# Kernel tuning notes

Hardware: AMD Instinct MI355X
Metric: run time of the kernel (lower is better)

Reference implementation:

```python
import jax, jax.numpy as jnp
import numpy as np

N_NODES = 50000
N_EDGES = 800000
NFEAT = 128
NHID = 64
NLAYER = 3
BN_EPS = 1e-5


def _bn(h, gamma, beta):
    # BatchNorm1d, training-mode batch statistics (biased variance)
    mu = jnp.mean(h, axis=0)
    var = jnp.mean((h - mu) ** 2, axis=0)
    return gamma * (h - mu) * jax.lax.rsqrt(var + BN_EPS) + beta


def setup_inputs() -> dict:
    key = jax.random.key(0)
    ks = jax.random.split(key, 8)
    x = jax.random.normal(ks[0], (N_NODES, NFEAT), dtype=jnp.float32)
    edge_index = jax.random.randint(ks[1], (2, N_EDGES), 0, N_NODES, dtype=jnp.int64)
    # transform: Linear(nfeat, nhid) with bias, then BN
    W_t = jax.random.normal(ks[2], (NFEAT, NHID), dtype=jnp.float32) / np.sqrt(NFEAT)
    b_t = jnp.zeros((NHID,), dtype=jnp.float32)
    g_t = jnp.ones((NHID,), dtype=jnp.float32)
    bb_t = jnp.zeros((NHID,), dtype=jnp.float32)
    # per-layer GIN MLPs (bias=False) and BN affine params, stacked over layers
    W1 = jax.random.normal(ks[3], (NLAYER, NHID, NHID), dtype=jnp.float32) / np.sqrt(NHID)
    W2 = jax.random.normal(ks[4], (NLAYER, NHID, NHID), dtype=jnp.float32) / np.sqrt(NHID)
    gamma = jnp.ones((NLAYER, NHID), dtype=jnp.float32)
    beta = jnp.zeros((NLAYER, NHID), dtype=jnp.float32)
    return {"x": x, "edge_index": edge_index, "W_t": W_t, "b_t": b_t,
            "g_t": g_t, "bb_t": bb_t, "W1": W1, "W2": W2,
            "gamma": gamma, "beta": beta}


def reference(x, edge_index, W_t, b_t, g_t, bb_t, W1, W2, gamma, beta):
    src, dst = edge_index[0], edge_index[1]
    # input transform: Linear + BN
    h = _bn(x @ W_t + b_t, g_t, bb_t)
    for i in range(NLAYER):
        # dropout p=0 -> identity
        # GINConv (eps=0): (1+eps)*h + sum_{j->i} h_j, then 2-layer MLP
        agg = h + jax.ops.segment_sum(h[src], dst, num_segments=N_NODES)
        h = jax.nn.relu(agg @ W1[i]) @ W2[i]
        h = jax.nn.relu(h)
        h = _bn(h, gamma[i], beta[i])
    # per-graph boolean-mask split is a pure partition of rows; return full matrix
    return h
```

## Files before the change

kernel.cpp:

```cpp
#include <hip/hip_runtime.h>

#define NND 50000
#define NED 800000
#define NF  128
#define NH  64
#define BN_EPS 1e-5
#define NCOPY 8
#define SCB  256
#define NSB  ((NND + SCB - 1) / SCB)
#define XNODES (NND / 8)
#define FCH  196
#define NT   782
#define PGRID (FCH * 8)

#define WS_HB     0
#define WS_AGG    6400000
#define WS_STATS  12800000
#define WS_DEG    (WS_STATS + 4*NCOPY*128*4)
#define WS_OFFS   (WS_DEG + NND*4)
#define WS_CUR    (WS_OFFS + (NND+4)*4)
#define WS_PARTS  (WS_CUR + NND*4)
#define WS_ESRC   (WS_PARTS + 256*4)

__device__ __forceinline__ unsigned bfrn(float x) {
    unsigned u = __float_as_uint(x);
    return (u + 0x7fffu + ((u >> 16) & 1u)) >> 16;
}
__device__ __forceinline__ unsigned pk(float lo, float hi) {
    return bfrn(lo) | (bfrn(hi) << 16);
}
__device__ __forceinline__ void upadd(unsigned u, float& lo, float& hi) {
    lo += __uint_as_float(u << 16);
    hi += __uint_as_float(u & 0xffff0000u);
}
__device__ __forceinline__ float ulo(unsigned u) { return __uint_as_float(u << 16); }
__device__ __forceinline__ float uhi(unsigned u) { return __uint_as_float(u & 0xffff0000u); }

__device__ __forceinline__ void bn_derive(const float* __restrict__ st, int c,
                                          const float* __restrict__ g,
                                          const float* __restrict__ b,
                                          float& sc, float& sh) {
    float sum = 0.f, ssq = 0.f;
#pragma unroll
    for (int cp = 0; cp < NCOPY; ++cp) {
        sum += st[cp * 128 + c];
        ssq += st[cp * 128 + 64 + c];
    }
    double mu  = (double)sum / (double)NND;
    double var = (double)ssq / (double)NND - mu * mu;
    if (var < 0.0) var = 0.0;
    double rs = 1.0 / sqrt(var + BN_EPS);
    double scd = (double)g[c] * rs;
    sc = (float)scd;
    sh = (float)((double)b[c] - mu * scd);
}

__global__ __launch_bounds__(256) void k_dtf(const int* __restrict__ dst,
                                             int* __restrict__ deg,
                                             const float* __restrict__ x,
                                             const float* __restrict__ Wt,
                                             const float* __restrict__ bt,
                                             unsigned* __restrict__ hB,
                                             float* __restrict__ stats) {
    __shared__ __align__(16) unsigned Wlu[NF * NH / 2];
    __shared__ __align__(16) float sT[64 * 68];
    int tid = threadIdx.x;

    if (blockIdx.x >= NT) {
        int dbid = blockIdx.x - NT;
        int xcd = dbid & 7;
        int chunk = dbid >> 3;
        int lo = xcd * XNODES;
        const int4* d4 = (const int4*)dst;
#pragma unroll
        for (int r = 0; r < 4; ++r) {
            int i = chunk * 1024 + r * 256 + tid;
            if (i < NED / 4) {
                int4 d = d4[i];
                if ((unsigned)(d.x - lo) < XNODES) atomicAdd(&deg[d.x], 1);
                if ((unsigned)(d.y - lo) < XNODES) atomicAdd(&deg[d.y], 1);
                if ((unsigned)(d.z - lo) < XNODES) atomicAdd(&deg[d.z], 1);
                if ((unsigned)(d.w - lo) < XNODES) atomicAdd(&deg[d.w], 1);
            }
        }
        return;
    }

    int tile = blockIdx.x;
    int base = tile * 64;
    const float4* x4 = (const float4*)x;

#pragma unroll
    for (int r = 0; r < 8; ++r) {
        int i4 = r * 256 + tid;
        float4 w = ((const float4*)Wt)[i4];
        uint2 wp; wp.x = pk(w.x, w.y); wp.y = pk(w.z, w.w);
        ((uint2*)Wlu)[i4] = wp;
    }

    int wave = tid >> 6, lane = tid & 63;
    int ti = lane & 7, tj = lane >> 3;
    int cw = wave * 32 + tj * 4;

    float acc[8][4];
#pragma unroll
    for (int i = 0; i < 8; ++i)
#pragma unroll
        for (int j = 0; j < 4; ++j) acc[i][j] = 0.f;

    for (int ch = 0; ch < 2; ++ch) {
        __syncthreads();
        float4 pf[4];
#pragma unroll
        for (int s = 0; s < 4; ++s) {
            int flat = s * 256 + tid;
            int nl = flat >> 4, q = flat & 15;
            pf[s] = make_float4(0.f, 0.f, 0.f, 0.f);
            if (base + nl < NND) pf[s] = x4[(size_t)(base + nl) * 32 + ch * 16 + q];
        }
#pragma unroll
        for (int s = 0; s < 4; ++s) {
            int flat = s * 256 + tid;
            int nl = flat >> 4, q = flat & 15;
            sT[(q * 4 + 0) * 68 + nl] = pf[s].x;
            sT[(q * 4 + 1) * 68 + nl] = pf[s].y;
            sT[(q * 4 + 2) * 68 + nl] = pf[s].z;
            sT[(q * 4 + 3) * 68 + nl] = pf[s].w;
        }
        __syncthreads();
        if (tid < 128) {
#pragma unroll 4
            for (int k = 0; k < 64; ++k) {
                const float* ap = &sT[k * 68 + ti * 8];
                float4 alo = *(const float4*)ap;
                float4 ahi = *(const float4*)(ap + 4);
                uint2 wu = *(const uint2*)&Wlu[(ch * 64 + k) * 32 + (cw >> 1)];
                float a8[8] = {alo.x, alo.y, alo.z, alo.w, ahi.x, ahi.y, ahi.z, ahi.w};
                float w4[4] = {ulo(wu.x), uhi(wu.x), ulo(wu.y), uhi(wu.y)};
#pragma unroll
                for (int i = 0; i < 8; ++i)
#pragma unroll
                    for (int j = 0; j < 4; ++j) acc[i][j] += a8[i] * w4[j];
            }
        }
    }
    if (tid >= 128) return;

    float4 bv = *(const float4*)&bt[cw];
    float bj[4] = {bv.x, bv.y, bv.z, bv.w};

    float s4[4] = {0.f, 0.f, 0.f, 0.f}, q4[4] = {0.f, 0.f, 0.f, 0.f};
    uint2* hB2 = (uint2*)hB;
#pragma unroll
    for (int i = 0; i < 8; ++i) {
        int n = base + ti * 8 + i;
        if (n < NND) {
            float o[4];
#pragma unroll
            for (int j = 0; j < 4; ++j) {
                o[j] = acc[i][j] + bj[j];
                s4[j] += o[j];
                q4[j] += o[j] * o[j];
            }
            uint2 ov; ov.x = pk(o[0], o[1]); ov.y = pk(o[2], o[3]);
            hB2[(size_t)n * 16 + wave * 8 + tj] = ov;
        }
    }
#pragma unroll
    for (int m = 1; m < 8; m <<= 1) {
#pragma unroll
        for (int j = 0; j < 4; ++j) {
            s4[j] += __shfl_xor(s4[j], m);
            q4[j] += __shfl_xor(q4[j], m);
        }
    }
    if (ti == 0) {
        int slot = (tile & (NCOPY - 1)) * 128;
#pragma unroll
        for (int j = 0; j < 4; ++j) {
            atomicAdd(&stats[slot + cw + j], s4[j]);
            atomicAdd(&stats[slot + 64 + cw + j], q4[j]);
        }
    }
}

__global__ __launch_bounds__(256) void k_fill(const int* __restrict__ src,
                                              const int* __restrict__ dst,
                                              int* __restrict__ cur,
                                              int* __restrict__ esrc) {
    int xcd = blockIdx.x & 7;
    int chunk = blockIdx.x >> 3;
    int lo = xcd * XNODES;
    const int4* d4 = (const int4*)dst;
    const int4* s4 = (const int4*)src;
#pragma unroll
    for (int r = 0; r < 4; ++r) {
        int i = chunk * 1024 + r * 256 + threadIdx.x;
        if (i < NED / 4) {
            int4 d = d4[i];
            int4 s = s4[i];
            if ((unsigned)(d.x - lo) < XNODES) esrc[atomicAdd(&cur[d.x], 1)] = s.x;
            if ((unsigned)(d.y - lo) < XNODES) esrc[atomicAdd(&cur[d.y], 1)] = s.y;
            if ((unsigned)(d.z - lo) < XNODES) esrc[atomicAdd(&cur[d.z], 1)] = s.z;
            if ((unsigned)(d.w - lo) < XNODES) esrc[atomicAdd(&cur[d.w], 1)] = s.w;
        }
    }
}

__global__ __launch_bounds__(SCB) void k_part(const int* __restrict__ deg,
                                              int* __restrict__ offs,
                                              int* __restrict__ parts) {
    __shared__ int sd[SCB];
    int t = threadIdx.x;
    int i = blockIdx.x * SCB + t;
    int v = (i < NND) ? deg[i] : 0;
    sd[t] = v;
    __syncthreads();
#pragma unroll
    for (int off = 1; off < SCB; off <<= 1) {
        int u = (t >= off) ? sd[t - off] : 0;
        __syncthreads();
        sd[t] += u;
        __syncthreads();
    }
    if (i < NND) offs[i] = sd[t] - v;
    if (t == SCB - 1) parts[blockIdx.x] = sd[t];
}

__global__ __launch_bounds__(256) void k_scan2(int* __restrict__ parts) {
    __shared__ int sd[256];
    int t = threadIdx.x;
    int v = (t < NSB) ? parts[t] : 0;
    sd[t] = v;
    __syncthreads();
#pragma unroll
    for (int off = 1; off < 256; off <<= 1) {
        int u = (t >= off) ? sd[t - off] : 0;
        __syncthreads();
        sd[t] += u;
        __syncthreads();
    }
    if (t < NSB) parts[t] = sd[t] - v;
}

__global__ __launch_bounds__(256) void k_apply(int* __restrict__ offs,
                                               const int* __restrict__ parts,
                                               int* __restrict__ cur) {
    int i = blockIdx.x * 256 + threadIdx.x;
    if (i < NND) {
        int o = offs[i] + parts[i >> 8];
        offs[i] = o;
        cur[i] = o;
    }
    if (i == NND) offs[NND] = NED;
}

__global__ __launch_bounds__(256) void k_agg(const uint4* __restrict__ hB4,
                                             uint4* __restrict__ aggB4,
                                             const float* __restrict__ stats,
                                             const float* __restrict__ g,
                                             const float* __restrict__ b,
                                             const int* __restrict__ offs,
                                             const int* __restrict__ esrc) {
    int tid  = threadIdx.x;
    int lane = tid & 63;
    int wv   = tid >> 6;
    int n = blockIdx.x * 4 + wv;
    int q = lane & 7;
    int r = lane >> 3;

    float scl, shl;
    bn_derive(stats, lane, g, b, scl, shl);

    int e0 = offs[n], e1 = offs[n + 1];
    int deg = e1 - e0;

    float a[8];
#pragma unroll
    for (int i = 0; i < 8; ++i) a[i] = 0.f;

    if (r == 0) {
        uint4 u = hB4[(size_t)n * 8 + q];
        upadd(u.x, a[0], a[1]); upadd(u.y, a[2], a[3]);
        upadd(u.z, a[4], a[5]); upadd(u.w, a[6], a[7]);
    }

    for (int bb = e0; bb < e1; bb += 64) {
        int m = e1 - bb; if (m > 64) m = 64;
        int idx = (lane < m) ? esrc[bb + lane] : 0;
        int t = 0;
        for (; t + 32 <= m; t += 32) {
            int j0 = __shfl(idx, t + r);
            int j1 = __shfl(idx, t + 8 + r);
            int j2 = __shfl(idx, t + 16 + r);
            int j3 = __shfl(idx, t + 24 + r);
            uint4 u0 = hB4[(size_t)j0 * 8 + q];
            uint4 u1 = hB4[(size_t)j1 * 8 + q];
            uint4 u2 = hB4[(size_t)j2 * 8 + q];
            uint4 u3 = hB4[(size_t)j3 * 8 + q];
            upadd(u0.x, a[0], a[1]); upadd(u0.y, a[2], a[3]);
            upadd(u0.z, a[4], a[5]); upadd(u0.w, a[6], a[7]);
            upadd(u1.x, a[0], a[1]); upadd(u1.y, a[2], a[3]);
            upadd(u1.z, a[4], a[5]); upadd(u1.w, a[6], a[7]);
            upadd(u2.x, a[0], a[1]); upadd(u2.y, a[2], a[3]);
            upadd(u2.z, a[4], a[5]); upadd(u2.w, a[6], a[7]);
            upadd(u3.x, a[0], a[1]); upadd(u3.y, a[2], a[3]);
            upadd(u3.z, a[4], a[5]); upadd(u3.w, a[6], a[7]);
        }
        for (; t < m; t += 8) {
            int e = t + r;
            int j = __shfl(idx, e & 63);
            if (e < m) {
                uint4 u = hB4[(size_t)j * 8 + q];
                upadd(u.x, a[0], a[1]); upadd(u.y, a[2], a[3]);
                upadd(u.z, a[4], a[5]); upadd(u.w, a[6], a[7]);
            }
        }
    }

#pragma unroll
    for (int msk = 8; msk <= 32; msk <<= 1)
#pragma unroll
        for (int i = 0; i < 8; ++i) a[i] += __shfl_xor(a[i], msk);

    float sc8[8], sh8[8];
#pragma unroll
    for (int j = 0; j < 8; ++j) {
        sc8[j] = __shfl(scl, q * 8 + j);
        sh8[j] = __shfl(shl, q * 8 + j);
    }

    if (r == 0) {
        float dn = (float)(deg + 1);
        float o[8];
#pragma unroll
        for (int j = 0; j < 8; ++j) o[j] = sc8[j] * a[j] + dn * sh8[j];
        uint4 ov;
        ov.x = pk(o[0], o[1]); ov.y = pk(o[2], o[3]);
        ov.z = pk(o[4], o[5]); ov.w = pk(o[6], o[7]);
        aggB4[(size_t)n * 8 + q] = ov;
    }
}

__global__ __launch_bounds__(128) void k_mlp(const uint4* __restrict__ aggB4,
                                             float* __restrict__ outF,
                                             unsigned* __restrict__ hBo,
                                             float* __restrict__ stats,
                                             const float* __restrict__ W1,
                                             const float* __restrict__ W2) {
    __shared__ __align__(16) float W1l[NH * NH];
    __shared__ __align__(16) float W2l[NH * NH];
    __shared__ __align__(16) float sT[64 * 68];
    int tid  = threadIdx.x;
    int wave = tid >> 6, lane = tid & 63;
    int ti = lane & 7, tj = lane >> 3;
    int tile = blockIdx.x;
    int base = tile * 64;
    int cw = wave * 32 + tj * 4;

#pragma unroll
    for (int r = 0; r < 8; ++r) {
        int i4 = r * 128 + tid;
        ((float4*)W1l)[i4] = ((const float4*)W1)[i4];
        ((float4*)W2l)[i4] = ((const float4*)W2)[i4];
    }
#pragma unroll
    for (int s = 0; s < 4; ++s) {
        int i4 = s * 128 + tid;
        int nl = i4 >> 3, q = i4 & 7;
        uint4 u = make_uint4(0u, 0u, 0u, 0u);
        if (base + nl < NND) u = aggB4[(size_t)(base + nl) * 8 + q];
        sT[(q * 8 + 0) * 68 + nl] = ulo(u.x);
        sT[(q * 8 + 1) * 68 + nl] = uhi(u.x);
        sT[(q * 8 + 2) * 68 + nl] = ulo(u.y);
        sT[(q * 8 + 3) * 68 + nl] = uhi(u.y);
        sT[(q * 8 + 4) * 68 + nl] = ulo(u.z);
        sT[(q * 8 + 5) * 68 + nl] = uhi(u.z);
        sT[(q * 8 + 6) * 68 + nl] = ulo(u.w);
        sT[(q * 8 + 7) * 68 + nl] = uhi(u.w);
    }
    __syncthreads();

    float a1[8][4];
#pragma unroll
    for (int i = 0; i < 8; ++i)
#pragma unroll
        for (int j = 0; j < 4; ++j) a1[i][j] = 0.f;
#pragma unroll 4
    for (int k = 0; k < 64; ++k) {
        const float* ap = &sT[k * 68 + ti * 8];
        float4 alo = *(const float4*)ap;
        float4 ahi = *(const float4*)(ap + 4);
        float4 wv  = *(const float4*)&W1l[k * NH + cw];
        float a8[8] = {alo.x, alo.y, alo.z, alo.w, ahi.x, ahi.y, ahi.z, ahi.w};
        float w4[4] = {wv.x, wv.y, wv.z, wv.w};
#pragma unroll
        for (int i = 0; i < 8; ++i)
#pragma unroll
            for (int j = 0; j < 4; ++j) a1[i][j] += a8[i] * w4[j];
    }
#pragma unroll
    for (int i = 0; i < 8; ++i)
#pragma unroll
        for (int j = 0; j < 4; ++j) a1[i][j] = fmaxf(a1[i][j], 0.f);

    __syncthreads();
#pragma unroll
    for (int j = 0; j < 4; ++j) {
        float* p = &sT[(cw + j) * 68 + ti * 8];
        float4 lo = {a1[0][j], a1[1][j], a1[2][j], a1[3][j]};
        float4 hi = {a1[4][j], a1[5][j], a1[6][j], a1[7][j]};
        *(float4*)p = lo;
        *(float4*)(p + 4) = hi;
    }
    __syncthreads();

    float a2[8][4];
#pragma unroll
    for (int i = 0; i < 8; ++i)
#pragma unroll
        for (int j = 0; j < 4; ++j) a2[i][j] = 0.f;
#pragma unroll 4
    for (int k = 0; k < 64; ++k) {
        const float* ap = &sT[k * 68 + ti * 8];
        float4 alo = *(const float4*)ap;
        float4 ahi = *(const float4*)(ap + 4);
        float4 wv  = *(const float4*)&W2l[k * NH + cw];
        float a8[8] = {alo.x, alo.y, alo.z, alo.w, ahi.x, ahi.y, ahi.z, ahi.w};
        float w4[4] = {wv.x, wv.y, wv.z, wv.w};
#pragma unroll
        for (int i = 0; i < 8; ++i)
#pragma unroll
            for (int j = 0; j < 4; ++j) a2[i][j] += a8[i] * w4[j];
    }

    float s4[4] = {0.f, 0.f, 0.f, 0.f}, q4[4] = {0.f, 0.f, 0.f, 0.f};
    uint2* hBo2 = (uint2*)hBo;
#pragma unroll
    for (int i = 0; i < 8; ++i) {
        int n = base + ti * 8 + i;
        if (n < NND) {
            float o[4];
#pragma unroll
            for (int j = 0; j < 4; ++j) {
                o[j] = fmaxf(a2[i][j], 0.f);
                s4[j] += o[j];
                q4[j] += o[j] * o[j];
            }
            if (outF) *(float4*)&outF[(size_t)n * NH + cw] = *(float4*)&o[0];
            if (hBo) {
                uint2 ov; ov.x = pk(o[0], o[1]); ov.y = pk(o[2], o[3]);
                hBo2[(size_t)n * 16 + wave * 8 + tj] = ov;
            }
        }
    }
#pragma unroll
    for (int m = 1; m < 8; m <<= 1) {
#pragma unroll
        for (int j = 0; j < 4; ++j) {
            s4[j] += __shfl_xor(s4[j], m);
            q4[j] += __shfl_xor(q4[j], m);
        }
    }
    if (ti == 0) {
        int slot = (tile & (NCOPY - 1)) * 128;
#pragma unroll
        for (int j = 0; j < 4; ++j) {
            atomicAdd(&stats[slot + cw + j], s4[j]);
            atomicAdd(&stats[slot + 64 + cw + j], q4[j]);
        }
    }
}

__global__ __launch_bounds__(256) void k_bnout(float* __restrict__ h,
                                               const float* __restrict__ stats,
                                               const float* __restrict__ g,
                                               const float* __restrict__ b) {
    __shared__ float sl[128];
    int tid = threadIdx.x;
    if (tid < 64) {
        float sc, sh;
        bn_derive(stats, tid, g, b, sc, sh);
        sl[tid]      = sc;
        sl[64 + tid] = sh;
    }
    __syncthreads();
    int i4 = blockIdx.x * 256 + tid;
    if (i4 < NND * NH / 4) {
        int cg = i4 & 15;
        float4 v   = ((float4*)h)[i4];
        float4 scv = *(float4*)&sl[cg * 4];
        float4 shv = *(float4*)&sl[64 + cg * 4];
        v.x = v.x * scv.x + shv.x;
        v.y = v.y * scv.y + shv.y;
        v.z = v.z * scv.z + shv.z;
        v.w = v.w * scv.w + shv.w;
        ((float4*)h)[i4] = v;
    }
}

extern "C" void kernel_launch(void* const* d_in, const int* in_sizes, int n_in,
                              void* d_out, int out_size, void* d_ws, size_t ws_size,
                              hipStream_t stream) {
    const float* x     = (const float*)d_in[0];
    const int*   ei    = (const int*)d_in[1];
    const float* Wt    = (const float*)d_in[2];
    const float* bt    = (const float*)d_in[3];
    const float* gt    = (const float*)d_in[4];
    const float* bbt   = (const float*)d_in[5];
    const float* W1    = (const float*)d_in[6];
    const float* W2    = (const float*)d_in[7];
    const float* gamma = (const float*)d_in[8];
    const float* beta  = (const float*)d_in[9];
    float* out = (float*)d_out;

    char* ws = (char*)d_ws;
    unsigned* hB    = (unsigned*)(ws + WS_HB);
    unsigned* aggB  = (unsigned*)(ws + WS_AGG);
    float*    stats = (float*)(ws + WS_STATS);
    int*      deg   = (int*)(ws + WS_DEG);
    int*      offs  = (int*)(ws + WS_OFFS);
    int*      cur   = (int*)(ws + WS_CUR);
    int*      parts = (int*)(ws + WS_PARTS);
    int*      esrc  = (int*)(ws + WS_ESRC);

    float* st0 = stats;
    float* st1 = stats + NCOPY * 128;
    float* st2 = stats + 2 * NCOPY * 128;
    float* st3 = stats + 3 * NCOPY * 128;

    const int* srcv = ei;
    const int* dstv = ei + NED;

    hipMemsetAsync(stats, 0, 4 * NCOPY * 128 * 4 + NND * 4, stream);

    k_dtf<<<NT + PGRID, 256, 0, stream>>>(dstv, deg, x, Wt, bt, hB, st0);
    k_part<<<NSB, SCB, 0, stream>>>(deg, offs, parts);
    k_scan2<<<1, 256, 0, stream>>>(parts);
    k_apply<<<NSB, 256, 0, stream>>>(offs, parts, cur);
    k_fill<<<PGRID, 256, 0, stream>>>(srcv, dstv, cur, esrc);

    const int NB = NND / 4;

    k_agg<<<NB, 256, 0, stream>>>((const uint4*)hB, (uint4*)aggB, st0, gt, bbt, offs, esrc);
    k_mlp<<<NT, 128, 0, stream>>>((const uint4*)aggB, nullptr, hB, st1, W1, W2);

    k_agg<<<NB, 256, 0, stream>>>((const uint4*)hB, (uint4*)aggB, st1, gamma, beta, offs, esrc);
    k_mlp<<<NT, 128, 0, stream>>>((const uint4*)aggB, nullptr, hB, st2, W1 + 4096, W2 + 4096);

    k_agg<<<NB, 256, 0, stream>>>((const uint4*)hB, (uint4*)aggB, st2, gamma + 64, beta + 64, offs, esrc);
    k_mlp<<<NT, 128, 0, stream>>>((const uint4*)aggB, out, nullptr, st3, W1 + 8192, W2 + 8192);

    k_bnout<<<(NND * NH / 4 + 255) / 256, 256, 0, stream>>>(out, st3, gamma + 128, beta + 128);
}
```

Baseline: 301.2 us.

## Batch edge loads before atomics and widen per-lane gathers in aggregation

The degree-count and CSR-fill kernels now issue all four int4 loads first, then do the atomics. Out-of-range indices are clamped instead of branched around, which lets the loads overlap. The aggregation kernel assigns 16 features (two uint4) per lane across 16 edge rows instead of 8. It issues all gathers for a 64-edge batch up front, with masked-weight FMAs replacing the scalar tail loop. This raises memory-level parallelism in the gather, at the cost of more registers, one more shuffle-reduction step, and wasted loads for padded edges.

```diff
diff --git a/kernel.cpp b/kernel.cpp
--- a/kernel.cpp
+++ b/kernel.cpp
@@ -12,6 +12,7 @@
 #define FCH  196
 #define NT   782
 #define PGRID (FCH * 8)
+#define NE4  (NED / 4)
 
 #define WS_HB     0
 #define WS_AGG    6400000
@@ -29,12 +30,14 @@
 __device__ __forceinline__ unsigned pk(float lo, float hi) {
     return bfrn(lo) | (bfrn(hi) << 16);
 }
-__device__ __forceinline__ void upadd(unsigned u, float& lo, float& hi) {
-    lo += __uint_as_float(u << 16);
-    hi += __uint_as_float(u & 0xffff0000u);
-}
 __device__ __forceinline__ float ulo(unsigned u) { return __uint_as_float(u << 16); }
 __device__ __forceinline__ float uhi(unsigned u) { return __uint_as_float(u & 0xffff0000u); }
+__device__ __forceinline__ void upadd(unsigned u, float& lo, float& hi) {
+    lo += ulo(u); hi += uhi(u);
+}
+__device__ __forceinline__ void upaddw(unsigned u, float w, float& lo, float& hi) {
+    lo = fmaf(w, ulo(u), lo); hi = fmaf(w, uhi(u), hi);
+}
 
 __device__ __forceinline__ void bn_derive(const float* __restrict__ st, int c,
                                           const float* __restrict__ g,
@@ -72,16 +75,20 @@
         int chunk = dbid >> 3;
         int lo = xcd * XNODES;
         const int4* d4 = (const int4*)dst;
+        int4 d[4];
 #pragma unroll
         for (int r = 0; r < 4; ++r) {
             int i = chunk * 1024 + r * 256 + tid;
-            if (i < NED / 4) {
-                int4 d = d4[i];
-                if ((unsigned)(d.x - lo) < XNODES) atomicAdd(&deg[d.x], 1);
-                if ((unsigned)(d.y - lo) < XNODES) atomicAdd(&deg[d.y], 1);
-                if ((unsigned)(d.z - lo) < XNODES) atomicAdd(&deg[d.z], 1);
-                if ((unsigned)(d.w - lo) < XNODES) atomicAdd(&deg[d.w], 1);
-            }
+            int ii = i < NE4 ? i : NE4 - 1;
+            d[r] = d4[ii];
+            if (i >= NE4) d[r] = make_int4(-1, -1, -1, -1);
+        }
+#pragma unroll
+        for (int r = 0; r < 4; ++r) {
+            if ((unsigned)(d[r].x - lo) < XNODES) atomicAdd(&deg[d[r].x], 1);
+            if ((unsigned)(d[r].y - lo) < XNODES) atomicAdd(&deg[d[r].y], 1);
+            if ((unsigned)(d[r].z - lo) < XNODES) atomicAdd(&deg[d[r].z], 1);
+            if ((unsigned)(d[r].w - lo) < XNODES) atomicAdd(&deg[d[r].w], 1);
         }
         return;
     }
@@ -193,17 +200,21 @@
     int lo = xcd * XNODES;
     const int4* d4 = (const int4*)dst;
     const int4* s4 = (const int4*)src;
+    int4 d[4], s[4];
 #pragma unroll
     for (int r = 0; r < 4; ++r) {
         int i = chunk * 1024 + r * 256 + threadIdx.x;
-        if (i < NED / 4) {
-            int4 d = d4[i];
-            int4 s = s4[i];
-            if ((unsigned)(d.x - lo) < XNODES) esrc[atomicAdd(&cur[d.x], 1)] = s.x;
-            if ((unsigned)(d.y - lo) < XNODES) esrc[atomicAdd(&cur[d.y], 1)] = s.y;
-            if ((unsigned)(d.z - lo) < XNODES) esrc[atomicAdd(&cur[d.z], 1)] = s.z;
-            if ((unsigned)(d.w - lo) < XNODES) esrc[atomicAdd(&cur[d.w], 1)] = s.w;
-        }
+        int ii = i < NE4 ? i : NE4 - 1;
+        d[r] = d4[ii];
+        s[r] = s4[ii];
+        if (i >= NE4) d[r] = make_int4(-1, -1, -1, -1);
+    }
+#pragma unroll
+    for (int r = 0; r < 4; ++r) {
+        if ((unsigned)(d[r].x - lo) < XNODES) esrc[atomicAdd(&cur[d[r].x], 1)] = s[r].x;
+        if ((unsigned)(d[r].y - lo) < XNODES) esrc[atomicAdd(&cur[d[r].y], 1)] = s[r].y;
+        if ((unsigned)(d[r].z - lo) < XNODES) esrc[atomicAdd(&cur[d[r].z], 1)] = s[r].z;
+        if ((unsigned)(d[r].w - lo) < XNODES) esrc[atomicAdd(&cur[d[r].w], 1)] = s[r].w;
     }
 }
 
@@ -266,8 +277,8 @@
     int lane = tid & 63;
     int wv   = tid >> 6;
     int n = blockIdx.x * 4 + wv;
-    int q = lane & 7;
-    int r = lane >> 3;
+    int q2 = lane & 3;
+    int r  = lane >> 2;
 
     float scl, shl;
     bn_derive(stats, lane, g, b, scl, shl);
@@ -275,70 +286,71 @@
     int e0 = offs[n], e1 = offs[n + 1];
     int deg = e1 - e0;
 
-    float a[8];
-#pragma unroll
-    for (int i = 0; i < 8; ++i) a[i] = 0.f;
+    float a[16];
+#pragma unroll
+    for (int i = 0; i < 16; ++i) a[i] = 0.f;
 
     if (r == 0) {
-        uint4 u = hB4[(size_t)n * 8 + q];
-        upadd(u.x, a[0], a[1]); upadd(u.y, a[2], a[3]);
-        upadd(u.z, a[4], a[5]); upadd(u.w, a[6], a[7]);
+        uint4 ua = hB4[(size_t)n * 8 + q2 * 2];
+        uint4 ub = hB4[(size_t)n * 8 + q2 * 2 + 1];
+        upadd(ua.x, a[0], a[1]);  upadd(ua.y, a[2], a[3]);
+        upadd(ua.z, a[4], a[5]);  upadd(ua.w, a[6], a[7]);
+        upadd(ub.x, a[8], a[9]);  upadd(ub.y, a[10], a[11]);
+        upadd(ub.z, a[12], a[13]); upadd(ub.w, a[14], a[15]);
     }
 
     for (int bb = e0; bb < e1; bb += 64) {
         int m = e1 - bb; if (m > 64) m = 64;
         int idx = (lane < m) ? esrc[bb + lane] : 0;
-        int t = 0;
-        for (; t + 32 <= m; t += 32) {
-            int j0 = __shfl(idx, t + r);
-            int j1 = __shfl(idx, t + 8 + r);
-            int j2 = __shfl(idx, t + 16 + r);
-            int j3 = __shfl(idx, t + 24 + r);
-            uint4 u0 = hB4[(size_t)j0 * 8 + q];
-            uint4 u1 = hB4[(size_t)j1 * 8 + q];
-            uint4 u2 = hB4[(size_t)j2 * 8 + q];
-            uint4 u3 = hB4[(size_t)j3 * 8 + q];
-            upadd(u0.x, a[0], a[1]); upadd(u0.y, a[2], a[3]);
-            upadd(u0.z, a[4], a[5]); upadd(u0.w, a[6], a[7]);
-            upadd(u1.x, a[0], a[1]); upadd(u1.y, a[2], a[3]);
-            upadd(u1.z, a[4], a[5]); upadd(u1.w, a[6], a[7]);
-            upadd(u2.x, a[0], a[1]); upadd(u2.y, a[2], a[3]);
-            upadd(u2.z, a[4], a[5]); upadd(u2.w, a[6], a[7]);
-            upadd(u3.x, a[0], a[1]); upadd(u3.y, a[2], a[3]);
-            upadd(u3.z, a[4], a[5]); upadd(u3.w, a[6], a[7]);
-        }
-        for (; t < m; t += 8) {
-            int e = t + r;
-            int j = __shfl(idx, e & 63);
-            if (e < m) {
-                uint4 u = hB4[(size_t)j * 8 + q];
-                upadd(u.x, a[0], a[1]); upadd(u.y, a[2], a[3]);
-                upadd(u.z, a[4], a[5]); upadd(u.w, a[6], a[7]);
+        int jj[4]; float w[4];
+        uint4 ua[4], ub[4];
+#pragma unroll
+        for (int gi = 0; gi < 4; ++gi) {
+            if (gi * 16 < m) {
+                int e = gi * 16 + r;
+                int ec = e < m ? e : m - 1;
+                jj[gi] = __shfl(idx, ec);
+                w[gi]  = e < m ? 1.f : 0.f;
+                ua[gi] = hB4[(size_t)jj[gi] * 8 + q2 * 2];
+                ub[gi] = hB4[(size_t)jj[gi] * 8 + q2 * 2 + 1];
             }
         }
-    }
-
-#pragma unroll
-    for (int msk = 8; msk <= 32; msk <<= 1)
-#pragma unroll
-        for (int i = 0; i < 8; ++i) a[i] += __shfl_xor(a[i], msk);
-
-    float sc8[8], sh8[8];
-#pragma unroll
-    for (int j = 0; j < 8; ++j) {
-        sc8[j] = __shfl(scl, q * 8 + j);
-        sh8[j] = __shfl(shl, q * 8 + j);
+#pragma unroll
+        for (int gi = 0; gi < 4; ++gi) {
+            if (gi * 16 < m) {
+                float wg = w[gi];
+                upaddw(ua[gi].x, wg, a[0], a[1]);   upaddw(ua[gi].y, wg, a[2], a[3]);
+                upaddw(ua[gi].z, wg, a[4], a[5]);   upaddw(ua[gi].w, wg, a[6], a[7]);
+                upaddw(ub[gi].x, wg, a[8], a[9]);   upaddw(ub[gi].y, wg, a[10], a[11]);
+                upaddw(ub[gi].z, wg, a[12], a[13]); upaddw(ub[gi].w, wg, a[14], a[15]);
+            }
+        }
+    }
+
+#pragma unroll
+    for (int msk = 4; msk <= 32; msk <<= 1)
+#pragma unroll
+        for (int i = 0; i < 16; ++i) a[i] += __shfl_xor(a[i], msk);
+
+    float sc16[16], sh16[16];
+#pragma unroll
+    for (int j = 0; j < 16; ++j) {
+        sc16[j] = __shfl(scl, q2 * 16 + j);
+        sh16[j] = __shfl(shl, q2 * 16 + j);
     }
 
     if (r == 0) {
         float dn = (float)(deg + 1);
-        float o[8];
-#pragma unroll
-        for (int j = 0; j < 8; ++j) o[j] = sc8[j] * a[j] + dn * sh8[j];
-        uint4 ov;
-        ov.x = pk(o[0], o[1]); ov.y = pk(o[2], o[3]);
-        ov.z = pk(o[4], o[5]); ov.w = pk(o[6], o[7]);
-        aggB4[(size_t)n * 8 + q] = ov;
+        float o[16];
+#pragma unroll
+        for (int j = 0; j < 16; ++j) o[j] = sc16[j] * a[j] + dn * sh16[j];
+        uint4 ova, ovb;
+        ova.x = pk(o[0], o[1]);   ova.y = pk(o[2], o[3]);
+        ova.z = pk(o[4], o[5]);   ova.w = pk(o[6], o[7]);
+        ovb.x = pk(o[8], o[9]);   ovb.y = pk(o[10], o[11]);
+        ovb.z = pk(o[12], o[13]); ovb.w = pk(o[14], o[15]);
+        aggB4[(size_t)n * 8 + q2 * 2]     = ova;
+        aggB4[(size_t)n * 8 + q2 * 2 + 1] = ovb;
     }
 }
 
```

Measured after the change: 363.4 us. 20.7% more time.
